# Kernel tuning notes

Hardware: AMD Instinct MI355X
Metric: run time of the kernel (lower is better)

The kernel has to match this reference:

```python
import jax, jax.numpy as jnp
import numpy as np

B, S, H = 4, 2048, 4096   # batch, seq, hidden
Q_DIM = 32 * 128          # num_attention_heads * head_dim
KV_DIM = 8 * 128          # num_key_value_heads * head_dim
R = 16                    # lora_r
SCALING = 32.0 / 16.0     # lora_alpha / lora_r


def setup_inputs() -> dict:
    key = jax.random.key(0)
    ks = jax.random.split(key, 10)
    def n(k, shape, scale):
        return jax.random.normal(k, shape, dtype=jnp.float32) * scale
    x = jax.random.normal(ks[0], (B, S, H), dtype=jnp.float32)
    # base weights stored as [out_dim, in_dim] like nn.Linear
    Wq = n(ks[1], (Q_DIM, H), 0.02)
    Wk = n(ks[2], (KV_DIM, H), 0.02)
    Wv = n(ks[3], (KV_DIM, H), 0.02)
    bq = n(ks[4], (Q_DIM,), 0.02)
    bk = n(ks[5], (KV_DIM,), 0.02)
    bv = n(ks[6], (KV_DIM,), 0.02)
    # LoRA A: kaiming-uniform-like init; B: zeros in training start, use small
    # random values here so the LoRA path is numerically exercised.
    bound = 1.0 / np.sqrt(H)
    Aq = jax.random.uniform(ks[7], (H, R), jnp.float32, -bound, bound)
    Ak = jax.random.uniform(ks[8], (H, R), jnp.float32, -bound, bound)
    Av = jax.random.uniform(ks[9], (H, R), jnp.float32, -bound, bound)
    kb = jax.random.split(jax.random.fold_in(key, 1), 3)
    Bq = n(kb[0], (R, Q_DIM), 0.01)
    Bk = n(kb[1], (R, KV_DIM), 0.01)
    Bv = n(kb[2], (R, KV_DIM), 0.01)
    return {"x": x, "Wq": Wq, "Wk": Wk, "Wv": Wv, "bq": bq, "bk": bk, "bv": bv,
            "Aq": Aq, "Bq": Bq, "Ak": Ak, "Bk": Bk, "Av": Av, "Bv": Bv}


def _proj(x, W, b, A, Bm):
    # base GEMM + low-rank LoRA delta + bias (dropout p=0 -> identity)
    base = jnp.einsum('bsh,oh->bso', x, W)
    delta = jnp.einsum('bsr,ro->bso', jnp.einsum('bsh,hr->bsr', x, A), Bm)
    return base + SCALING * delta + b


def reference(x, Wq, Wk, Wv, bq, bk, bv, Aq, Bq, Ak, Bk, Av, Bv):
    q = _proj(x, Wq, bq, Aq, Bq)  # [B,S,Q_DIM]
    k = _proj(x, Wk, bk, Ak, Bk)  # [B,S,KV_DIM]
    v = _proj(x, Wv, bv, Av, Bv)  # [B,S,KV_DIM]
    return q, k, v
```

## Files before the change

### kernel.cpp

```cpp
#include <hip/hip_runtime.h>


#define GLOBAL_AS __attribute__((address_space(1)))
#define LDS_AS    __attribute__((address_space(3)))

typedef __attribute__((ext_vector_type(8))) short  short8;
typedef __attribute__((ext_vector_type(4))) float  floatx4;

constexpr int Mdim = 8192;
constexpr int Kdim = 4096;
constexpr int NQ   = 4096;
constexpr int NKV  = 1024;
constexpr int NTOT = NQ + 2 * NKV;
constexpr float LORA_SCALE = 2.0f;

constexpr int BM = 256, BN = 256;
constexpr int TILES_M = Mdim / BM;
constexpr int TILES_N = NTOT / BN;
constexpr int NWG = TILES_M * TILES_N;
constexpr int NSLICE = Kdim / 32;

constexpr int WEFF_BLOCKS = (NTOT / 64) * (Kdim / 512);
constexpr int CVT_BLOCKS  = 2048;
constexpr int AT_STRIDE   = 516;

__device__ __forceinline__ unsigned short f2bf(float f) {
    union { float f; unsigned int u; } a; a.f = f;
    unsigned int r = a.u + 0x7FFFu + ((a.u >> 16) & 1u);
    return (unsigned short)(r >> 16);
}

__global__ __launch_bounds__(256)
void prep_kernel(const float4* __restrict__ x4, unsigned short* __restrict__ Xbf,
                 const float* __restrict__ Wq, const float* __restrict__ Wk,
                 const float* __restrict__ Wv,
                 const float* __restrict__ Aq, const float* __restrict__ Bq,
                 const float* __restrict__ Ak, const float* __restrict__ Bk,
                 const float* __restrict__ Av, const float* __restrict__ Bv,
                 unsigned short* __restrict__ Wf) {
    __shared__ float AsT[16 * AT_STRIDE];
    __shared__ float Bsc[64 * 16];

    const int tid = threadIdx.x;

    if (blockIdx.x >= WEFF_BLOCKS) {
        int i = (blockIdx.x - WEFF_BLOCKS) * 256 + tid;
        const int stride = CVT_BLOCKS * 256;
        const int n4 = Mdim * Kdim / 4;
        ushort4* out = (ushort4*)Xbf;
        for (; i < n4; i += stride) {
            float4 v = x4[i];
            ushort4 u;
            u.x = f2bf(v.x); u.y = f2bf(v.y); u.z = f2bf(v.z); u.w = f2bf(v.w);
            out[i] = u;
        }
        return;
    }

    const int n0 = (blockIdx.x >> 3) * 64;
    const int h0 = (blockIdx.x & 7) * 512;

    const float* W; const float* A; const float* Bm; int O; int nn0;
    if (n0 < NQ)            { W = Wq; A = Aq; Bm = Bq; O = NQ;  nn0 = n0; }
    else if (n0 < NQ + NKV) { W = Wk; A = Ak; Bm = Bk; O = NKV; nn0 = n0 - NQ; }
    else                    { W = Wv; A = Av; Bm = Bv; O = NKV; nn0 = n0 - NQ - NKV; }

    {
        const float4* Af4 = (const float4*)(A) + h0 * 4;
        #pragma unroll
        for (int i = 0; i < 8; ++i) {
            const int f = i * 256 + tid;
            const float4 v = Af4[f];
            const int hl = f >> 2;
            const int r0 = (f & 3) * 4;
            AsT[(r0 + 0) * AT_STRIDE + hl] = v.x;
            AsT[(r0 + 1) * AT_STRIDE + hl] = v.y;
            AsT[(r0 + 2) * AT_STRIDE + hl] = v.z;
            AsT[(r0 + 3) * AT_STRIDE + hl] = v.w;
        }
    }
    {
        const int nl = tid & 63;
        const int rq = tid >> 6;
        #pragma unroll
        for (int j = 0; j < 4; ++j) {
            const int r = rq * 4 + j;
            Bsc[nl * 16 + r] = Bm[r * O + nn0 + nl] * LORA_SCALE;
        }
    }
    __syncthreads();

    const int wv_ = tid >> 6;
    const int lane = tid & 63;

    #pragma unroll
    for (int pass = 0; pass < 2; ++pass) {
        const int hl = pass * 256 + lane * 4;
        float4 areg[16];
        #pragma unroll
        for (int r = 0; r < 16; ++r)
            areg[r] = *(const float4*)(&AsT[r * AT_STRIDE + hl]);

        for (int i = 0; i < 16; ++i) {
            const int nl = wv_ * 16 + i;
            const float4 w4 = *(const float4*)(W + (size_t)(nn0 + nl) * Kdim + h0 + hl);
            const float4* b4 = (const float4*)(&Bsc[nl * 16]);
            float4 d = {0.f, 0.f, 0.f, 0.f};
            #pragma unroll
            for (int q = 0; q < 4; ++q) {
                const float4 b = b4[q];
                d.x += areg[q*4+0].x * b.x + areg[q*4+1].x * b.y + areg[q*4+2].x * b.z + areg[q*4+3].x * b.w;
                d.y += areg[q*4+0].y * b.x + areg[q*4+1].y * b.y + areg[q*4+2].y * b.z + areg[q*4+3].y * b.w;
                d.z += areg[q*4+0].z * b.x + areg[q*4+1].z * b.y + areg[q*4+2].z * b.z + areg[q*4+3].z * b.w;
                d.w += areg[q*4+0].w * b.x + areg[q*4+1].w * b.y + areg[q*4+2].w * b.z + areg[q*4+3].w * b.w;
            }
            ushort4 u;
            u.x = f2bf(w4.x + d.x); u.y = f2bf(w4.y + d.y);
            u.z = f2bf(w4.z + d.z); u.w = f2bf(w4.w + d.w);
            *(ushort4*)(Wf + (size_t)(n0 + nl) * Kdim + h0 + hl) = u;
        }
    }
}

__global__ __launch_bounds__(512, 2)
void gemm_qkv_kernel(const unsigned short* __restrict__ X,
                     const unsigned short* __restrict__ Wf,
                     const float* __restrict__ bq, const float* __restrict__ bk,
                     const float* __restrict__ bv,
                     float* __restrict__ out) {
    __shared__ __align__(16) unsigned short Abuf[4][8192];
    __shared__ __align__(16) unsigned short Bbuf[4][8192];

    const int tid  = threadIdx.x;
    const int lane = tid & 63;
    const int w    = tid >> 6;
    const int wr   = w >> 2;
    const int wc   = w & 3;

    int bid = blockIdx.x;
    bid = (bid & 7) * (NWG / 8) + (bid >> 3);
    const int row0 = (bid / TILES_N) * BM;
    const int col0 = (bid % TILES_N) * BN;

    const int swz    = (((lane >> 4) ^ ((lane >> 1) & 3)) << 4);
    const int aByte0 = (wr * 128 + (lane & 15)) * 64 + swz;
    const int bByte0 = (wc * 64  + (lane & 15)) * 64 + swz;

    const int srow = (w << 4) + (lane >> 2);
    const int kswz = (((lane & 3) ^ ((lane >> 3) & 3)) << 3);
    const unsigned short* pA0 = X  + (size_t)(row0 + srow) * Kdim + kswz;
    const unsigned short* pA1 = pA0 + (size_t)128 * Kdim;
    const unsigned short* pB0 = Wf + (size_t)(col0 + srow) * Kdim + kswz;
    const unsigned short* pB1 = pB0 + (size_t)128 * Kdim;

    floatx4 acc[8][4];
    #pragma unroll
    for (int i = 0; i < 8; ++i)
        #pragma unroll
        for (int j = 0; j < 4; ++j)
            acc[i][j] = (floatx4){0.f, 0.f, 0.f, 0.f};

    short8 bf[4];

#define STAGE(MATA, SS)                                                          \
    { const int ss_ = (SS); const int st_ = (SS) & 3;                            \
      if (MATA) {                                                                \
        __builtin_amdgcn_global_load_lds((const GLOBAL_AS void*)(pA0 + ss_ * 32),\
            (LDS_AS void*)(&Abuf[st_][w * 512]),        16, 0, 0);               \
        __builtin_amdgcn_global_load_lds((const GLOBAL_AS void*)(pA1 + ss_ * 32),\
            (LDS_AS void*)(&Abuf[st_][4096 + w * 512]), 16, 0, 0);               \
      } else {                                                                   \
        __builtin_amdgcn_global_load_lds((const GLOBAL_AS void*)(pB0 + ss_ * 32),\
            (LDS_AS void*)(&Bbuf[st_][w * 512]),        16, 0, 0);               \
        __builtin_amdgcn_global_load_lds((const GLOBAL_AS void*)(pB1 + ss_ * 32),\
            (LDS_AS void*)(&Bbuf[st_][4096 + w * 512]), 16, 0, 0);               \
      } }

#define DO_PHASE(G, MH, DOSTAGE, SMATA, SS, WAITMODE)                            \
    {                                                                            \
      const int slot_ = (G) & 3;                                                 \
      const char* abase_ = (const char*)Abuf + slot_ * 16384;                    \
      short8 af[4];                                                              \
      _Pragma("unroll")                                                          \
      for (int mf = 0; mf < 4; ++mf)                                             \
        af[mf] = *(const short8*)(abase_ + aByte0 + ((MH) * 4 + mf) * 1024);     \
      if ((MH) == 0) {                                                           \
        const char* bbase_ = (const char*)Bbuf + slot_ * 16384;                  \
        _Pragma("unroll")                                                        \
        for (int nf = 0; nf < 4; ++nf)                                           \
          bf[nf] = *(const short8*)(bbase_ + bByte0 + nf * 1024);                \
      }                                                                          \
      if (DOSTAGE) STAGE(SMATA, SS);                                             \
      __builtin_amdgcn_s_barrier();                                              \
      asm volatile("s_waitcnt lgkmcnt(0)");                                      \
      __builtin_amdgcn_s_setprio(1);                                             \
      _Pragma("unroll")                                                          \
      for (int mf = 0; mf < 4; ++mf)                                             \
        _Pragma("unroll")                                                        \
        for (int nf = 0; nf < 4; ++nf)                                           \
          acc[(MH) * 4 + mf][nf] = __builtin_amdgcn_mfma_f32_16x16x32_bf16(      \
              af[mf], bf[nf], acc[(MH) * 4 + mf][nf], 0, 0, 0);                  \
      __builtin_amdgcn_s_setprio(0);                                             \
      if ((WAITMODE) == 1) asm volatile("s_waitcnt vmcnt(4)" ::: "memory");      \
      if ((WAITMODE) == 2) asm volatile("s_waitcnt vmcnt(0)" ::: "memory");      \
      __builtin_amdgcn_s_barrier();                                              \
    }

    STAGE(1, 0); STAGE(0, 0);
    STAGE(1, 1); STAGE(0, 1);
    STAGE(1, 2); STAGE(0, 2);
    asm volatile("s_waitcnt vmcnt(4)" ::: "memory");
    __builtin_amdgcn_s_barrier();

    for (int j = 0; j < NSLICE / 4 - 1; ++j) {
        const int g0 = j * 4;
        DO_PHASE(g0 + 0, 0, 1, 1, g0 + 3, 0);
        DO_PHASE(g0 + 0, 1, 1, 0, g0 + 3, 0);
        DO_PHASE(g0 + 1, 0, 1, 1, g0 + 4, 0);
        DO_PHASE(g0 + 1, 1, 1, 0, g0 + 4, 1);
        DO_PHASE(g0 + 2, 0, 1, 1, g0 + 5, 0);
        DO_PHASE(g0 + 2, 1, 1, 0, g0 + 5, 0);
        DO_PHASE(g0 + 3, 0, 1, 1, g0 + 6, 0);
        DO_PHASE(g0 + 3, 1, 1, 0, g0 + 6, 1);
    }
    DO_PHASE(124, 0, 1, 1, 127, 0);
    DO_PHASE(124, 1, 1, 0, 127, 0);
    DO_PHASE(125, 0, 0, 0, 0,   0);
    DO_PHASE(125, 1, 0, 0, 0,   1);
    DO_PHASE(126, 0, 0, 0, 0,   0);
    DO_PHASE(126, 1, 0, 0, 0,   2);
    DO_PHASE(127, 0, 0, 0, 0,   0);
    DO_PHASE(127, 1, 0, 0, 0,   0);

#undef DO_PHASE
#undef STAGE

    float* obase; int ldo; const float* bias; int cofs;
    if (col0 < NQ) {
        obase = out;                             ldo = NQ;  bias = bq; cofs = 0;
    } else if (col0 < NQ + NKV) {
        obase = out + (size_t)Mdim * NQ;         ldo = NKV; bias = bk; cofs = NQ;
    } else {
        obase = out + (size_t)Mdim * (NQ + NKV); ldo = NKV; bias = bv; cofs = NQ + NKV;
    }

    #pragma unroll
    for (int nf = 0; nf < 4; ++nf) {
        const int col = col0 + wc * 64 + nf * 16 + (lane & 15) - cofs;
        const float b = bias[col];
        #pragma unroll
        for (int mf = 0; mf < 8; ++mf) {
            #pragma unroll
            for (int r = 0; r < 4; ++r) {
                const int row = row0 + wr * 128 + mf * 16 + (lane >> 4) * 4 + r;
                obase[(size_t)row * ldo + col] = acc[mf][nf][r] + b;
            }
        }
    }
}

extern "C" void kernel_launch(void* const* d_in, const int* in_sizes, int n_in,
                              void* d_out, int out_size, void* d_ws, size_t ws_size,
                              hipStream_t stream) {
    const float* x  = (const float*)d_in[0];
    const float* Wq = (const float*)d_in[1];
    const float* Wk = (const float*)d_in[2];
    const float* Wv = (const float*)d_in[3];
    const float* bq = (const float*)d_in[4];
    const float* bk = (const float*)d_in[5];
    const float* bv = (const float*)d_in[6];
    const float* Aq = (const float*)d_in[7];
    const float* Bq = (const float*)d_in[8];
    const float* Ak = (const float*)d_in[9];
    const float* Bk = (const float*)d_in[10];
    const float* Av = (const float*)d_in[11];
    const float* Bv = (const float*)d_in[12];
    float* out = (float*)d_out;

    unsigned short* Xbf = (unsigned short*)d_ws;
    unsigned short* Wf  = Xbf + (size_t)Mdim * Kdim;

    prep_kernel<<<WEFF_BLOCKS + CVT_BLOCKS, 256, 0, stream>>>(
        (const float4*)x, Xbf, Wq, Wk, Wv, Aq, Bq, Ak, Bk, Av, Bv, Wf);

    gemm_qkv_kernel<<<NWG, 512, 0, stream>>>(Xbf, Wf, bq, bk, bv, out);
}
```

Before: 461.5 us.

## Software-pipeline LDS fragment reads with double-buffered registers in GEMM main loop

```diff
diff --git a/kernel.cpp b/kernel.cpp
--- a/kernel.cpp
+++ b/kernel.cpp
@@ -160,79 +160,87 @@
         for (int j = 0; j < 4; ++j)
             acc[i][j] = (floatx4){0.f, 0.f, 0.f, 0.f};
 
-    short8 bf[4];
-
-#define STAGE(MATA, SS)                                                          \
-    { const int ss_ = (SS); const int st_ = (SS) & 3;                            \
+    short8 afr[2][4];
+    short8 bfr[2][4];
+
+#define STAGE(MATA, SS, SLOT)                                                    \
+    { const int ss_ = (SS);                                                      \
       if (MATA) {                                                                \
         __builtin_amdgcn_global_load_lds((const GLOBAL_AS void*)(pA0 + ss_ * 32),\
-            (LDS_AS void*)(&Abuf[st_][w * 512]),        16, 0, 0);               \
+            (LDS_AS void*)(&Abuf[SLOT][w * 512]),        16, 0, 0);              \
         __builtin_amdgcn_global_load_lds((const GLOBAL_AS void*)(pA1 + ss_ * 32),\
-            (LDS_AS void*)(&Abuf[st_][4096 + w * 512]), 16, 0, 0);               \
+            (LDS_AS void*)(&Abuf[SLOT][4096 + w * 512]), 16, 0, 0);              \
       } else {                                                                   \
         __builtin_amdgcn_global_load_lds((const GLOBAL_AS void*)(pB0 + ss_ * 32),\
-            (LDS_AS void*)(&Bbuf[st_][w * 512]),        16, 0, 0);               \
+            (LDS_AS void*)(&Bbuf[SLOT][w * 512]),        16, 0, 0);              \
         __builtin_amdgcn_global_load_lds((const GLOBAL_AS void*)(pB1 + ss_ * 32),\
-            (LDS_AS void*)(&Bbuf[st_][4096 + w * 512]), 16, 0, 0);               \
+            (LDS_AS void*)(&Bbuf[SLOT][4096 + w * 512]), 16, 0, 0);              \
       } }
 
-#define DO_PHASE(G, MH, DOSTAGE, SMATA, SS, WAITMODE)                            \
-    {                                                                            \
-      const int slot_ = (G) & 3;                                                 \
-      const char* abase_ = (const char*)Abuf + slot_ * 16384;                    \
-      short8 af[4];                                                              \
+#define READA(P, SLOT, MH)                                                       \
+    { const char* ab_ = (const char*)Abuf + (SLOT) * 16384;                      \
       _Pragma("unroll")                                                          \
       for (int mf = 0; mf < 4; ++mf)                                             \
-        af[mf] = *(const short8*)(abase_ + aByte0 + ((MH) * 4 + mf) * 1024);     \
-      if ((MH) == 0) {                                                           \
-        const char* bbase_ = (const char*)Bbuf + slot_ * 16384;                  \
-        _Pragma("unroll")                                                        \
-        for (int nf = 0; nf < 4; ++nf)                                           \
-          bf[nf] = *(const short8*)(bbase_ + bByte0 + nf * 1024);                \
-      }                                                                          \
-      if (DOSTAGE) STAGE(SMATA, SS);                                             \
-      __builtin_amdgcn_s_barrier();                                              \
-      asm volatile("s_waitcnt lgkmcnt(0)");                                      \
-      __builtin_amdgcn_s_setprio(1);                                             \
+        afr[P][mf] = *(const short8*)(ab_ + aByte0 + ((MH) * 4 + mf) * 1024); }
+
+#define READB(P, SLOT)                                                           \
+    { const char* bb_ = (const char*)Bbuf + (SLOT) * 16384;                      \
+      _Pragma("unroll")                                                          \
+      for (int nf = 0; nf < 4; ++nf)                                             \
+        bfr[P][nf] = *(const short8*)(bb_ + bByte0 + nf * 1024); }
+
+#define MFMA16(PA, PB, MH)                                                       \
+    { __builtin_amdgcn_s_setprio(1);                                             \
       _Pragma("unroll")                                                          \
       for (int mf = 0; mf < 4; ++mf)                                             \
         _Pragma("unroll")                                                        \
         for (int nf = 0; nf < 4; ++nf)                                           \
           acc[(MH) * 4 + mf][nf] = __builtin_amdgcn_mfma_f32_16x16x32_bf16(      \
-              af[mf], bf[nf], acc[(MH) * 4 + mf][nf], 0, 0, 0);                  \
-      __builtin_amdgcn_s_setprio(0);                                             \
-      if ((WAITMODE) == 1) asm volatile("s_waitcnt vmcnt(4)" ::: "memory");      \
-      if ((WAITMODE) == 2) asm volatile("s_waitcnt vmcnt(0)" ::: "memory");      \
-      __builtin_amdgcn_s_barrier();                                              \
-    }
-
-    STAGE(1, 0); STAGE(0, 0);
-    STAGE(1, 1); STAGE(0, 1);
-    STAGE(1, 2); STAGE(0, 2);
-    asm volatile("s_waitcnt vmcnt(4)" ::: "memory");
+              afr[PA][mf], bfr[PB][nf], acc[(MH) * 4 + mf][nf], 0, 0, 0);        \
+      __builtin_amdgcn_s_setprio(0); }
+
+#define PHASE(PAC, PBC, MH, PRA, NAP, NSLOT, NMH, PRB, NBP, DOST, SM, SS, SSLOT, WM, BAR) \
+    { if (PRA) READA(NAP, NSLOT, NMH);                                           \
+      if (PRB) READB(NBP, NSLOT);                                                \
+      if (DOST) STAGE(SM, SS, SSLOT);                                            \
+      MFMA16(PAC, PBC, MH);                                                      \
+      if ((WM) == 1) asm volatile("s_waitcnt vmcnt(6)" ::: "memory");            \
+      if ((WM) == 2) asm volatile("s_waitcnt vmcnt(4)" ::: "memory");            \
+      if ((WM) == 3) asm volatile("s_waitcnt vmcnt(0)" ::: "memory");            \
+      if (BAR) __builtin_amdgcn_s_barrier(); }
+
+    STAGE(1, 0, 0); STAGE(0, 0, 0);
+    STAGE(1, 1, 1); STAGE(0, 1, 1);
+    STAGE(1, 2, 2); STAGE(0, 2, 2);
+    asm volatile("s_waitcnt vmcnt(8)" ::: "memory");
     __builtin_amdgcn_s_barrier();
+    READA(0, 0, 0);
+    READB(0, 0);
 
     for (int j = 0; j < NSLICE / 4 - 1; ++j) {
-        const int g0 = j * 4;
-        DO_PHASE(g0 + 0, 0, 1, 1, g0 + 3, 0);
-        DO_PHASE(g0 + 0, 1, 1, 0, g0 + 3, 0);
-        DO_PHASE(g0 + 1, 0, 1, 1, g0 + 4, 0);
-        DO_PHASE(g0 + 1, 1, 1, 0, g0 + 4, 1);
-        DO_PHASE(g0 + 2, 0, 1, 1, g0 + 5, 0);
-        DO_PHASE(g0 + 2, 1, 1, 0, g0 + 5, 0);
-        DO_PHASE(g0 + 3, 0, 1, 1, g0 + 6, 0);
-        DO_PHASE(g0 + 3, 1, 1, 0, g0 + 6, 1);
-    }
-    DO_PHASE(124, 0, 1, 1, 127, 0);
-    DO_PHASE(124, 1, 1, 0, 127, 0);
-    DO_PHASE(125, 0, 0, 0, 0,   0);
-    DO_PHASE(125, 1, 0, 0, 0,   1);
-    DO_PHASE(126, 0, 0, 0, 0,   0);
-    DO_PHASE(126, 1, 0, 0, 0,   2);
-    DO_PHASE(127, 0, 0, 0, 0,   0);
-    DO_PHASE(127, 1, 0, 0, 0,   0);
-
-#undef DO_PHASE
+        const int g = j * 4;
+        PHASE(0,  0,  0,  1,  1,  0,    1,  0,  0,   1,   1,  g + 3, 3,    1, 1);
+        PHASE(1,  0,  1,  1,  0,  1,    0,  1,  1,   1,   0,  g + 3, 3,    0, 1);
+        PHASE(0,  1,  0,  1,  1,  1,    1,  0,  0,   1,   1,  g + 4, 0,    1, 1);
+        PHASE(1,  1,  1,  1,  0,  2,    0,  1,  0,   1,   0,  g + 4, 0,    0, 1);
+        PHASE(0,  0,  0,  1,  1,  2,    1,  0,  0,   1,   1,  g + 5, 1,    1, 1);
+        PHASE(1,  0,  1,  1,  0,  3,    0,  1,  1,   1,   0,  g + 5, 1,    0, 1);
+        PHASE(0,  1,  0,  1,  1,  3,    1,  0,  0,   1,   1,  g + 6, 2,    1, 1);
+        PHASE(1,  1,  1,  1,  0,  0,    0,  1,  0,   1,   0,  g + 6, 2,    0, 1);
+    }
+    PHASE(0, 0, 0,  1, 1, 0, 1,  0, 0,  1, 1, 127, 3,  1, 1);
+    PHASE(1, 0, 1,  1, 0, 1, 0,  1, 1,  1, 0, 127, 3,  0, 1);
+    PHASE(0, 1, 0,  1, 1, 1, 1,  0, 0,  0, 0, 0,   0,  2, 1);
+    PHASE(1, 1, 1,  1, 0, 2, 0,  1, 0,  0, 0, 0,   0,  0, 1);
+    PHASE(0, 0, 0,  1, 1, 2, 1,  0, 0,  0, 0, 0,   0,  3, 1);
+    PHASE(1, 0, 1,  1, 0, 3, 0,  1, 1,  0, 0, 0,   0,  0, 1);
+    PHASE(0, 1, 0,  1, 1, 3, 1,  0, 0,  0, 0, 0,   0,  0, 1);
+    PHASE(1, 1, 1,  0, 0, 0, 0,  0, 0,  0, 0, 0,   0,  0, 0);
+
+#undef PHASE
+#undef MFMA16
+#undef READB
+#undef READA
 #undef STAGE
 
     float* obase; int ldo; const float* bias; int cofs;
```

New measurement: 472.9 us. +2.5%, slower.
